# Optimization experiments

Measured on AMD Instinct MI355X. Metric: run time of the kernel, lower is better.

Reference implementation:

```python
import jax, jax.numpy as jnp
import numpy as np

MAX_VAL = 1000000000000.0


def setup_inputs() -> dict:
    key = jax.random.key(0)
    k1, k2, k3, k4 = jax.random.split(key, 4)
    B, H, N, D = 2, 16, 2048, 64
    query = jax.random.normal(k1, (B, H, N, D), dtype=jnp.float32)
    key_t = jax.random.normal(k2, (B, H, N, D), dtype=jnp.float32)
    value = jax.random.normal(k3, (B, H, N, D), dtype=jnp.float32)
    mask = jax.random.randint(k4, (B, 1, 1, N), 0, 2).astype(bool)
    return {"query": query, "key": key_t, "value": value, "mask": mask,
            "global_num": 8, "window_size": 64}


def reference(query, key, value, mask, global_num, window_size):
    # query/key/value: [B, H, N, D]; mask: [B, 1, 1, N] bool (True = keep)
    B, H, N, D = query.shape
    scale = 1.0 / jnp.sqrt(jnp.asarray(D, dtype=query.dtype))

    # split heads: first global_num are global, rest are local (windowed)
    q_g, k_g, v_g = query[:, :global_num], key[:, :global_num], value[:, :global_num]
    q_l, k_l, v_l = query[:, global_num:], key[:, global_num:], value[:, global_num:]

    # ---- global heads: dense masked attention ----
    scores_g = jnp.einsum('bhqd,bhkd->bhqk', q_g, k_g) * scale
    scores_g = jnp.where(mask, scores_g, -MAX_VAL)
    p_g = jax.nn.softmax(scores_g, axis=-1)
    out_g = jnp.einsum('bhqk,bhkd->bhqd', p_g, v_l[:, :0]) if False else jnp.einsum('bhqk,bhkd->bhqd', p_g, v_g)

    # ---- local heads: window-banded mask on top of padding mask ----
    pos = jnp.arange(N)
    distance = jnp.abs(pos[None, :] - pos[:, None])  # [N, N]
    band = (distance <= window_size)                 # [N, N] bool
    mask_l = mask & band                             # [B, 1, N, N]
    scores_l = jnp.einsum('bhqd,bhkd->bhqk', q_l, k_l) * scale
    scores_l = jnp.where(mask_l, scores_l, -MAX_VAL)
    p_l = jax.nn.softmax(scores_l, axis=-1)
    out_l = jnp.einsum('bhqk,bhkd->bhqd', p_l, v_l)

    out = jnp.concatenate([out_g, out_l], axis=1)  # [B, H, N, D]
    return (out, p_g, p_l)
```

## Files before the change

### kernel.cpp

```cpp
#include <hip/hip_runtime.h>
#include <stdint.h>

typedef __attribute__((ext_vector_type(8))) __bf16 bf16x8;
typedef __attribute__((ext_vector_type(4))) float f32x4;
typedef __attribute__((ext_vector_type(4))) int i32x4;

#define DEVI static __device__ __forceinline__

constexpr int NN = 2048;
constexpr int DD = 64;
constexpr int NH = 16;
constexpr int NG = 8;
constexpr float SCALE = 0.125f;
constexpr float NEGBIG = -1.0e12f;
constexpr size_t OUT_ELEMS = (size_t)2 * NH * NN * DD;
constexpr size_t PG_ELEMS  = (size_t)2 * NG * NN * NN;

struct Frag { bf16x8 hi, lo; };

DEVI Frag make_frag(const float* p) {
  f32x4 a = *(const f32x4*)p;
  f32x4 b = *(const f32x4*)(p + 4);
  Frag f;
#pragma unroll
  for (int j = 0; j < 8; j++) {
    float x = (j < 4) ? a[j] : b[j - 4];
    __bf16 h = (__bf16)x;
    f.hi[j] = h;
    f.lo[j] = (__bf16)(x - (float)h);
  }
  return f;
}

DEVI f32x4 mfma(bf16x8 a, bf16x8 b, f32x4 c) {
  return __builtin_amdgcn_mfma_f32_16x16x32_bf16(a, b, c, 0, 0, 0);
}

DEVI void compute_st(const Frag kf[2][2], const Frag* qf_rs, f32x4 acc[2]) {
#pragma unroll
  for (int Mt = 0; Mt < 2; Mt++) {
    f32x4 c = {0.f, 0.f, 0.f, 0.f};
#pragma unroll
    for (int ks = 0; ks < 2; ks++) {
      c = mfma(kf[Mt][ks].hi, qf_rs[ks].hi, c);
      c = mfma(kf[Mt][ks].hi, qf_rs[ks].lo, c);
      c = mfma(kf[Mt][ks].lo, qf_rs[ks].hi, c);
    }
    acc[Mt] = c;
  }
}

__global__ __launch_bounds__(256, 2)
void wattn(const float* __restrict__ Q, const float* __restrict__ K,
           const float* __restrict__ V, const int* __restrict__ MSK,
           float* __restrict__ OUT) {
  const int bid = blockIdx.x;
  const bool loc = bid >= 256;
  const int lb = loc ? bid - 256 : bid;
  const int bh = lb >> 4;
  const int b  = bh >> 3;
  const int hh = bh & 7;
  const int h  = loc ? (hh + 8) : hh;
  const int wave = (int)(threadIdx.x >> 6);
  const int lane = (int)(threadIdx.x & 63);
  const int qi = lane >> 4;
  const int li = lane & 15;
  const int rb = (lb & 15) * 128 + wave * 32;

  const float* qp = Q + ((size_t)(b * NH + h) * NN) * DD;
  const float* kp = K + ((size_t)(b * NH + h) * NN) * DD;
  const float* vp = V + ((size_t)(b * NH + h) * NN) * DD;
  const int*   mp = MSK + (size_t)b * NN;
  float* op = OUT + ((size_t)(b * NH + h) * NN) * DD;
  float* pp = OUT + OUT_ELEMS + (loc ? PG_ELEMS : (size_t)0)
                  + ((size_t)(b * NG + hh) * NN) * NN;

  Frag qf[2][2];
#pragma unroll
  for (int rs = 0; rs < 2; rs++)
#pragma unroll
    for (int ks = 0; ks < 2; ks++)
      qf[rs][ks] = make_frag(qp + (size_t)(rb + rs * 16 + li) * DD + ks * 32 + qi * 8);

  int wlo = 0, whi = 0;
  if (loc) {
    wlo = rb - 64; if (wlo < 0) wlo = 0;
    whi = rb + 96; if (whi > NN) whi = NN;
    const f32x4 z = {0.f, 0.f, 0.f, 0.f};
#pragma unroll 1
    for (int rr = 0; rr < 32; rr++) {
      float* dst = pp + (size_t)(rb + rr) * NN;
#pragma unroll 1
      for (int c = lane * 4; c < NN; c += 256) {
        if (c >= wlo && c < whi) continue;
        *(f32x4*)(dst + c) = z;
      }
    }
  }

  const int ntiles = loc ? 5 : 64;

  float m[2] = {NEGBIG, NEGBIG};
  float l[2] = {0.f, 0.f};

#pragma unroll 1
  for (int t = 0; t < ntiles; t++) {
    const int wc = loc ? (rb - 64 + 32 * t) : (32 * t);
    if (wc < 0 || wc >= NN) continue;

    Frag kf[2][2];
#pragma unroll
    for (int Mt = 0; Mt < 2; Mt++)
#pragma unroll
      for (int ks = 0; ks < 2; ks++)
        kf[Mt][ks] = make_frag(kp + (size_t)(wc + Mt * 16 + li) * DD + ks * 32 + qi * 8);

    i32x4 mv[2];
    mv[0] = *(const i32x4*)(mp + wc + qi * 4);
    mv[1] = *(const i32x4*)(mp + wc + 16 + qi * 4);

#pragma unroll
    for (int rs = 0; rs < 2; rs++) {
      f32x4 acc[2];
      compute_st(kf, qf[rs], acc);
      const int row = rb + rs * 16 + li;
      float vals[8];
#pragma unroll
      for (int Mt = 0; Mt < 2; Mt++)
#pragma unroll
        for (int r = 0; r < 4; r++) {
          const int col = wc + Mt * 16 + qi * 4 + r;
          bool ok = (mv[Mt][r] != 0);
          if (loc) { int d = row - col; if (d < 0) d = -d; ok = ok && (d <= 64); }
          vals[Mt * 4 + r] = ok ? acc[Mt][r] * SCALE : NEGBIG;
        }
      float mx = vals[0];
#pragma unroll
      for (int j = 1; j < 8; j++) mx = fmaxf(mx, vals[j]);
      const float mn = fmaxf(m[rs], mx);
      float s = 0.f;
#pragma unroll
      for (int j = 0; j < 8; j++) s += __expf(vals[j] - mn);
      l[rs] = l[rs] * __expf(m[rs] - mn) + s;
      m[rs] = mn;
    }
  }

  float rl[2];
#pragma unroll
  for (int rs = 0; rs < 2; rs++) {
#pragma unroll
    for (int off = 16; off <= 32; off <<= 1) {
      const float mo = __shfl_xor(m[rs], off);
      const float lo2 = __shfl_xor(l[rs], off);
      const float mn = fmaxf(m[rs], mo);
      l[rs] = l[rs] * __expf(m[rs] - mn) + lo2 * __expf(mo - mn);
      m[rs] = mn;
    }
    rl[rs] = 1.0f / l[rs];
  }

  f32x4 o[2][4];
#pragma unroll
  for (int rs = 0; rs < 2; rs++)
#pragma unroll
    for (int dt = 0; dt < 4; dt++) o[rs][dt] = (f32x4){0.f, 0.f, 0.f, 0.f};

  const int srcA = (((qi * 2) + 0) & 3) * 16 + li;
  const int srcB = (((qi * 2) + 1) & 3) * 16 + li;
  const bool selB = (qi >> 1) != 0;

#pragma unroll 1
  for (int t = 0; t < ntiles; t++) {
    const int wc = loc ? (rb - 64 + 32 * t) : (32 * t);
    if (wc < 0 || wc >= NN) continue;

    Frag kf[2][2];
#pragma unroll
    for (int Mt = 0; Mt < 2; Mt++)
#pragma unroll
      for (int ks = 0; ks < 2; ks++)
        kf[Mt][ks] = make_frag(kp + (size_t)(wc + Mt * 16 + li) * DD + ks * 32 + qi * 8);

    i32x4 mv[2];
    mv[0] = *(const i32x4*)(mp + wc + qi * 4);
    mv[1] = *(const i32x4*)(mp + wc + 16 + qi * 4);

    bf16x8 vf[4];
#pragma unroll
    for (int dt = 0; dt < 4; dt++)
#pragma unroll
      for (int j = 0; j < 8; j++)
        vf[dt][j] = (__bf16)vp[(size_t)(wc + qi * 8 + j) * DD + dt * 16 + li];

#pragma unroll
    for (int rs = 0; rs < 2; rs++) {
      f32x4 acc[2];
      compute_st(kf, qf[rs], acc);
      const int row = rb + rs * 16 + li;
      float pf[8];
#pragma unroll
      for (int Mt = 0; Mt < 2; Mt++)
#pragma unroll
        for (int r = 0; r < 4; r++) {
          const int col = wc + Mt * 16 + qi * 4 + r;
          bool ok = (mv[Mt][r] != 0);
          if (loc) { int d = row - col; if (d < 0) d = -d; ok = ok && (d <= 64); }
          const float vv = ok ? acc[Mt][r] * SCALE : NEGBIG;
          pf[Mt * 4 + r] = __expf(vv - m[rs]) * rl[rs];
        }
      float pa[8];
#pragma unroll
      for (int j = 0; j < 8; j++) {
        const int src = (j < 4) ? srcA : srcB;
        const float v0 = __shfl(pf[0 + (j & 3)], src);
        const float v1 = __shfl(pf[4 + (j & 3)], src);
        pa[j] = selB ? v1 : v0;
      }
      float* prow = pp + (size_t)(rb + rs * 16 + li) * NN + wc + qi * 8;
      *(f32x4*)prow       = (f32x4){pa[0], pa[1], pa[2], pa[3]};
      *(f32x4*)(prow + 4) = (f32x4){pa[4], pa[5], pa[6], pa[7]};
      bf16x8 pb;
#pragma unroll
      for (int j = 0; j < 8; j++) pb[j] = (__bf16)pa[j];
#pragma unroll
      for (int dt = 0; dt < 4; dt++)
        o[rs][dt] = mfma(pb, vf[dt], o[rs][dt]);
    }
  }

#pragma unroll
  for (int rs = 0; rs < 2; rs++) {
#pragma unroll
    for (int dt = 0; dt < 4; dt++)
#pragma unroll
      for (int r = 0; r < 4; r++) {
        const int row = rb + rs * 16 + qi * 4 + r;
        op[(size_t)row * DD + dt * 16 + li] = o[rs][dt][r];
      }
  }
}

extern "C" void kernel_launch(void* const* d_in, const int* in_sizes, int n_in,
                              void* d_out, int out_size, void* d_ws, size_t ws_size,
                              hipStream_t stream) {
  (void)in_sizes; (void)n_in; (void)out_size; (void)d_ws; (void)ws_size;
  const float* Q = (const float*)d_in[0];
  const float* K = (const float*)d_in[1];
  const float* V = (const float*)d_in[2];
  const int*   M = (const int*)d_in[3];
  float* O = (float*)d_out;
  wattn<<<dim3(512), dim3(256), 0, stream>>>(Q, K, V, M, O);
}
```

Measured before the change: 754.5 us.

## Precompute bf16 hi/lo splits of Q/K and transposed bf16 V in workspace

Adds a prep kernel that converts Q and K into separate bf16 hi and lo arrays and writes a transposed bf16 copy of V into the workspace. The attention kernel then loads ready-made fragments with vector loads instead of redoing the float-to-bf16 split for every K tile, and replaces the strided scalar V gathers with contiguous loads. The cost is an extra launch and extra global traffic to write and re-read the workspace. The kernel falls back to the original path when the workspace is too small.

```diff
diff --git a/kernel.cpp b/kernel.cpp
--- a/kernel.cpp
+++ b/kernel.cpp
@@ -15,6 +15,8 @@
 constexpr float NEGBIG = -1.0e12f;
 constexpr size_t OUT_ELEMS = (size_t)2 * NH * NN * DD;
 constexpr size_t PG_ELEMS  = (size_t)2 * NG * NN * NN;
+constexpr size_t T_ELEMS   = (size_t)2 * NH * NN * DD;
+constexpr size_t WS_NEED   = 5 * T_ELEMS * sizeof(__bf16);
 
 struct Frag { bf16x8 hi, lo; };
 
@@ -50,10 +52,50 @@
   }
 }
 
+__global__ __launch_bounds__(256)
+void prep(const float* __restrict__ Q, const float* __restrict__ K,
+          const float* __restrict__ V, __bf16* __restrict__ W) {
+  const int bid = blockIdx.x;
+  if (bid < 4096) {
+    const float* src = (bid < 2048) ? Q : K;
+    __bf16* hi = W + ((bid < 2048) ? (size_t)0 : 2 * T_ELEMS);
+    __bf16* lo = hi + T_ELEMS;
+    const size_t base = ((size_t)(bid & 2047) * 256 + threadIdx.x) * 8;
+    f32x4 a = *(const f32x4*)(src + base);
+    f32x4 b = *(const f32x4*)(src + base + 4);
+    bf16x8 h, l;
+#pragma unroll
+    for (int j = 0; j < 8; j++) {
+      float x = (j < 4) ? a[j] : b[j - 4];
+      __bf16 hh = (__bf16)x;
+      h[j] = hh;
+      l[j] = (__bf16)(x - (float)hh);
+    }
+    *(bf16x8*)(hi + base) = h;
+    *(bf16x8*)(lo + base) = l;
+  } else {
+    __bf16* vt = W + 4 * T_ELEMS;
+    const int t  = (bid - 4096) * 256 + (int)threadIdx.x;
+    const int ng = t & 63;
+    const int dh = t >> 6;
+    const int d  = dh & 63;
+    const int bh = dh >> 6;
+    const float* vp = V + (size_t)bh * NN * DD;
+    __bf16* dst = vt + ((size_t)bh * DD + d) * NN + ng * 32;
+    bf16x8 o[4];
+#pragma unroll
+    for (int j = 0; j < 32; j++)
+      o[j >> 3][j & 7] = (__bf16)vp[(size_t)(ng * 32 + j) * DD + d];
+#pragma unroll
+    for (int k = 0; k < 4; k++) *(bf16x8*)(dst + k * 8) = o[k];
+  }
+}
+
+template <bool PRE>
 __global__ __launch_bounds__(256, 2)
 void wattn(const float* __restrict__ Q, const float* __restrict__ K,
            const float* __restrict__ V, const int* __restrict__ MSK,
-           float* __restrict__ OUT) {
+           float* __restrict__ OUT, const __bf16* __restrict__ W) {
   const int bid = blockIdx.x;
   const bool loc = bid >= 256;
   const int lb = loc ? bid - 256 : bid;
@@ -67,11 +109,17 @@
   const int li = lane & 15;
   const int rb = (lb & 15) * 128 + wave * 32;
 
-  const float* qp = Q + ((size_t)(b * NH + h) * NN) * DD;
-  const float* kp = K + ((size_t)(b * NH + h) * NN) * DD;
-  const float* vp = V + ((size_t)(b * NH + h) * NN) * DD;
+  const size_t tbase = ((size_t)(b * NH + h) * NN) * DD;
+  const float* qp = Q + tbase;
+  const float* kp = K + tbase;
+  const float* vp = V + tbase;
+  const __bf16* qhi = W + tbase;
+  const __bf16* qlo = W + T_ELEMS + tbase;
+  const __bf16* khi = W + 2 * T_ELEMS + tbase;
+  const __bf16* klo = W + 3 * T_ELEMS + tbase;
+  const __bf16* vt  = W + 4 * T_ELEMS + (size_t)(b * NH + h) * DD * NN;
   const int*   mp = MSK + (size_t)b * NN;
-  float* op = OUT + ((size_t)(b * NH + h) * NN) * DD;
+  float* op = OUT + tbase;
   float* pp = OUT + OUT_ELEMS + (loc ? PG_ELEMS : (size_t)0)
                   + ((size_t)(b * NG + hh) * NN) * NN;
 
@@ -79,8 +127,15 @@
 #pragma unroll
   for (int rs = 0; rs < 2; rs++)
 #pragma unroll
-    for (int ks = 0; ks < 2; ks++)
-      qf[rs][ks] = make_frag(qp + (size_t)(rb + rs * 16 + li) * DD + ks * 32 + qi * 8);
+    for (int ks = 0; ks < 2; ks++) {
+      const size_t off = (size_t)(rb + rs * 16 + li) * DD + ks * 32 + qi * 8;
+      if constexpr (PRE) {
+        qf[rs][ks].hi = *(const bf16x8*)(qhi + off);
+        qf[rs][ks].lo = *(const bf16x8*)(qlo + off);
+      } else {
+        qf[rs][ks] = make_frag(qp + off);
+      }
+    }
 
   int wlo = 0, whi = 0;
   if (loc) {
@@ -112,8 +167,15 @@
 #pragma unroll
     for (int Mt = 0; Mt < 2; Mt++)
 #pragma unroll
-      for (int ks = 0; ks < 2; ks++)
-        kf[Mt][ks] = make_frag(kp + (size_t)(wc + Mt * 16 + li) * DD + ks * 32 + qi * 8);
+      for (int ks = 0; ks < 2; ks++) {
+        const size_t off = (size_t)(wc + Mt * 16 + li) * DD + ks * 32 + qi * 8;
+        if constexpr (PRE) {
+          kf[Mt][ks].hi = *(const bf16x8*)(khi + off);
+          kf[Mt][ks].lo = *(const bf16x8*)(klo + off);
+        } else {
+          kf[Mt][ks] = make_frag(kp + off);
+        }
+      }
 
     i32x4 mv[2];
     mv[0] = *(const i32x4*)(mp + wc + qi * 4);
@@ -179,19 +241,32 @@
 #pragma unroll
     for (int Mt = 0; Mt < 2; Mt++)
 #pragma unroll
-      for (int ks = 0; ks < 2; ks++)
-        kf[Mt][ks] = make_frag(kp + (size_t)(wc + Mt * 16 + li) * DD + ks * 32 + qi * 8);
+      for (int ks = 0; ks < 2; ks++) {
+        const size_t off = (size_t)(wc + Mt * 16 + li) * DD + ks * 32 + qi * 8;
+        if constexpr (PRE) {
+          kf[Mt][ks].hi = *(const bf16x8*)(khi + off);
+          kf[Mt][ks].lo = *(const bf16x8*)(klo + off);
+        } else {
+          kf[Mt][ks] = make_frag(kp + off);
+        }
+      }
 
     i32x4 mv[2];
     mv[0] = *(const i32x4*)(mp + wc + qi * 4);
     mv[1] = *(const i32x4*)(mp + wc + 16 + qi * 4);
 
     bf16x8 vf[4];
-#pragma unroll
-    for (int dt = 0; dt < 4; dt++)
-#pragma unroll
-      for (int j = 0; j < 8; j++)
-        vf[dt][j] = (__bf16)vp[(size_t)(wc + qi * 8 + j) * DD + dt * 16 + li];
+    if constexpr (PRE) {
+#pragma unroll
+      for (int dt = 0; dt < 4; dt++)
+        vf[dt] = *(const bf16x8*)(vt + (size_t)(dt * 16 + li) * NN + wc + qi * 8);
+    } else {
+#pragma unroll
+      for (int dt = 0; dt < 4; dt++)
+#pragma unroll
+        for (int j = 0; j < 8; j++)
+          vf[dt][j] = (__bf16)vp[(size_t)(wc + qi * 8 + j) * DD + dt * 16 + li];
+    }
 
 #pragma unroll
     for (int rs = 0; rs < 2; rs++) {
@@ -244,11 +319,17 @@
 extern "C" void kernel_launch(void* const* d_in, const int* in_sizes, int n_in,
                               void* d_out, int out_size, void* d_ws, size_t ws_size,
                               hipStream_t stream) {
-  (void)in_sizes; (void)n_in; (void)out_size; (void)d_ws; (void)ws_size;
+  (void)in_sizes; (void)n_in; (void)out_size;
   const float* Q = (const float*)d_in[0];
   const float* K = (const float*)d_in[1];
   const float* V = (const float*)d_in[2];
   const int*   M = (const int*)d_in[3];
   float* O = (float*)d_out;
-  wattn<<<dim3(512), dim3(256), 0, stream>>>(Q, K, V, M, O);
-}
+  if (ws_size >= WS_NEED && d_ws != nullptr) {
+    __bf16* W = (__bf16*)d_ws;
+    prep<<<dim3(4608), dim3(256), 0, stream>>>(Q, K, V, W);
+    wattn<true><<<dim3(512), dim3(256), 0, stream>>>(Q, K, V, M, O, W);
+  } else {
+    wattn<false><<<dim3(512), dim3(256), 0, stream>>>(Q, K, V, M, O, nullptr);
+  }
+}
```

New measurement: 784.0 us. +3.9%, slower.

## Balance global and local head work per wave with 16-row jobs

Applied to the files above, without the earlier changes.

Each wave now handles 16 query rows instead of 32, and runs one global-head job followed by one local-head job for the same (b, head-index, rows), so every block carries equal work instead of separate light local blocks and heavy global blocks. Block IDs are remapped so consecutive blocks land on different XCDs. The local-head zero fill of the probability matrix moves into the second pass loop as tile-wise stores, which replaces the separate per-row strided zeroing. Halving rows per wave doubles the K/V fragment loads per query row, which raises global load traffic.

```diff
diff --git a/kernel.cpp b/kernel.cpp
--- a/kernel.cpp
+++ b/kernel.cpp
@@ -36,209 +36,190 @@
   return __builtin_amdgcn_mfma_f32_16x16x32_bf16(a, b, c, 0, 0, 0);
 }
 
-DEVI void compute_st(const Frag kf[2][2], const Frag* qf_rs, f32x4 acc[2]) {
+DEVI void compute_st(const Frag kf[2][2], const Frag qf[2], f32x4 acc[2]) {
 #pragma unroll
   for (int Mt = 0; Mt < 2; Mt++) {
     f32x4 c = {0.f, 0.f, 0.f, 0.f};
 #pragma unroll
     for (int ks = 0; ks < 2; ks++) {
-      c = mfma(kf[Mt][ks].hi, qf_rs[ks].hi, c);
-      c = mfma(kf[Mt][ks].hi, qf_rs[ks].lo, c);
-      c = mfma(kf[Mt][ks].lo, qf_rs[ks].hi, c);
+      c = mfma(kf[Mt][ks].hi, qf[ks].hi, c);
+      c = mfma(kf[Mt][ks].hi, qf[ks].lo, c);
+      c = mfma(kf[Mt][ks].lo, qf[ks].hi, c);
     }
     acc[Mt] = c;
   }
+}
+
+template <bool LOC>
+DEVI void attn_job(int bh, int r0, int lane,
+                   const float* __restrict__ Q, const float* __restrict__ K,
+                   const float* __restrict__ V, const int* __restrict__ MSK,
+                   float* __restrict__ OUT) {
+  const int b  = bh >> 3;
+  const int hh = bh & 7;
+  const int h  = LOC ? (hh + 8) : hh;
+  const int qi = lane >> 4;
+  const int li = lane & 15;
+
+  const size_t tb = ((size_t)(b * NH + h) * NN) * DD;
+  const float* qp = Q + tb;
+  const float* kp = K + tb;
+  const float* vp = V + tb;
+  const int*   mp = MSK + (size_t)b * NN;
+  float* op = OUT + tb;
+  float* pp = OUT + OUT_ELEMS + (LOC ? PG_ELEMS : (size_t)0)
+                  + ((size_t)(b * NG + hh) * NN) * NN;
+
+  Frag qf[2];
+#pragma unroll
+  for (int ks = 0; ks < 2; ks++)
+    qf[ks] = make_frag(qp + (size_t)(r0 + li) * DD + ks * 32 + qi * 8);
+
+  int cb = 0;
+  if constexpr (LOC) cb = (r0 - 64) & ~31;
+
+  float m = NEGBIG, l = 0.f;
+
+  const int ntA = LOC ? 5 : 64;
+#pragma unroll 1
+  for (int t = 0; t < ntA; t++) {
+    const int wc = LOC ? (cb + 32 * t) : (32 * t);
+    if (LOC && ((unsigned)wc >= (unsigned)NN)) continue;
+
+    Frag kf[2][2];
+#pragma unroll
+    for (int Mt = 0; Mt < 2; Mt++)
+#pragma unroll
+      for (int ks = 0; ks < 2; ks++)
+        kf[Mt][ks] = make_frag(kp + (size_t)(wc + Mt * 16 + li) * DD + ks * 32 + qi * 8);
+
+    i32x4 mv[2];
+    mv[0] = *(const i32x4*)(mp + wc + qi * 4);
+    mv[1] = *(const i32x4*)(mp + wc + 16 + qi * 4);
+
+    f32x4 acc[2];
+    compute_st(kf, qf, acc);
+    const int row = r0 + li;
+    float vals[8];
+#pragma unroll
+    for (int Mt = 0; Mt < 2; Mt++)
+#pragma unroll
+      for (int r = 0; r < 4; r++) {
+        const int col = wc + Mt * 16 + qi * 4 + r;
+        bool ok = (mv[Mt][r] != 0);
+        if constexpr (LOC) { int d = row - col; if (d < 0) d = -d; ok = ok && (d <= 64); }
+        vals[Mt * 4 + r] = ok ? acc[Mt][r] * SCALE : NEGBIG;
+      }
+    float mx = vals[0];
+#pragma unroll
+    for (int j = 1; j < 8; j++) mx = fmaxf(mx, vals[j]);
+    const float mn = fmaxf(m, mx);
+    float s = 0.f;
+#pragma unroll
+    for (int j = 0; j < 8; j++) s += __expf(vals[j] - mn);
+    l = l * __expf(m - mn) + s;
+    m = mn;
+  }
+
+#pragma unroll
+  for (int off = 16; off <= 32; off <<= 1) {
+    const float mo  = __shfl_xor(m, off);
+    const float lo2 = __shfl_xor(l, off);
+    const float mn  = fmaxf(m, mo);
+    l = l * __expf(m - mn) + lo2 * __expf(mo - mn);
+    m = mn;
+  }
+  const float rl = 1.0f / l;
+
+  f32x4 o[4];
+#pragma unroll
+  for (int dt = 0; dt < 4; dt++) o[dt] = (f32x4){0.f, 0.f, 0.f, 0.f};
+
+  const int srcA = (((qi * 2) + 0) & 3) * 16 + li;
+  const int srcB = (((qi * 2) + 1) & 3) * 16 + li;
+  const bool selB = (qi >> 1) != 0;
+
+#pragma unroll 1
+  for (int t = 0; t < 64; t++) {
+    const int wc = 32 * t;
+    float* prow = pp + (size_t)(r0 + li) * NN + wc + qi * 8;
+    if (LOC && ((unsigned)(wc - cb) >= 160u)) {
+      const f32x4 z = {0.f, 0.f, 0.f, 0.f};
+      *(f32x4*)prow       = z;
+      *(f32x4*)(prow + 4) = z;
+      continue;
+    }
+
+    Frag kf[2][2];
+#pragma unroll
+    for (int Mt = 0; Mt < 2; Mt++)
+#pragma unroll
+      for (int ks = 0; ks < 2; ks++)
+        kf[Mt][ks] = make_frag(kp + (size_t)(wc + Mt * 16 + li) * DD + ks * 32 + qi * 8);
+
+    i32x4 mv[2];
+    mv[0] = *(const i32x4*)(mp + wc + qi * 4);
+    mv[1] = *(const i32x4*)(mp + wc + 16 + qi * 4);
+
+    bf16x8 vf[4];
+#pragma unroll
+    for (int dt = 0; dt < 4; dt++)
+#pragma unroll
+      for (int j = 0; j < 8; j++)
+        vf[dt][j] = (__bf16)vp[(size_t)(wc + qi * 8 + j) * DD + dt * 16 + li];
+
+    f32x4 acc[2];
+    compute_st(kf, qf, acc);
+    const int row = r0 + li;
+    float pf[8];
+#pragma unroll
+    for (int Mt = 0; Mt < 2; Mt++)
+#pragma unroll
+      for (int r = 0; r < 4; r++) {
+        const int col = wc + Mt * 16 + qi * 4 + r;
+        bool ok = (mv[Mt][r] != 0);
+        if constexpr (LOC) { int d = row - col; if (d < 0) d = -d; ok = ok && (d <= 64); }
+        const float vv = ok ? acc[Mt][r] * SCALE : NEGBIG;
+        pf[Mt * 4 + r] = __expf(vv - m) * rl;
+      }
+    float pa[8];
+#pragma unroll
+    for (int j = 0; j < 8; j++) {
+      const int src = (j < 4) ? srcA : srcB;
+      const float v0 = __shfl(pf[0 + (j & 3)], src);
+      const float v1 = __shfl(pf[4 + (j & 3)], src);
+      pa[j] = selB ? v1 : v0;
+    }
+    *(f32x4*)prow       = (f32x4){pa[0], pa[1], pa[2], pa[3]};
+    *(f32x4*)(prow + 4) = (f32x4){pa[4], pa[5], pa[6], pa[7]};
+    bf16x8 pb;
+#pragma unroll
+    for (int j = 0; j < 8; j++) pb[j] = (__bf16)pa[j];
+#pragma unroll
+    for (int dt = 0; dt < 4; dt++)
+      o[dt] = mfma(pb, vf[dt], o[dt]);
+  }
+
+#pragma unroll
+  for (int dt = 0; dt < 4; dt++)
+#pragma unroll
+    for (int r = 0; r < 4; r++)
+      op[(size_t)(r0 + qi * 4 + r) * DD + dt * 16 + li] = o[dt][r];
 }
 
 __global__ __launch_bounds__(256, 2)
 void wattn(const float* __restrict__ Q, const float* __restrict__ K,
            const float* __restrict__ V, const int* __restrict__ MSK,
            float* __restrict__ OUT) {
-  const int bid = blockIdx.x;
-  const bool loc = bid >= 256;
-  const int lb = loc ? bid - 256 : bid;
-  const int bh = lb >> 4;
-  const int b  = bh >> 3;
-  const int hh = bh & 7;
-  const int h  = loc ? (hh + 8) : hh;
   const int wave = (int)(threadIdx.x >> 6);
   const int lane = (int)(threadIdx.x & 63);
-  const int qi = lane >> 4;
-  const int li = lane & 15;
-  const int rb = (lb & 15) * 128 + wave * 32;
-
-  const float* qp = Q + ((size_t)(b * NH + h) * NN) * DD;
-  const float* kp = K + ((size_t)(b * NH + h) * NN) * DD;
-  const float* vp = V + ((size_t)(b * NH + h) * NN) * DD;
-  const int*   mp = MSK + (size_t)b * NN;
-  float* op = OUT + ((size_t)(b * NH + h) * NN) * DD;
-  float* pp = OUT + OUT_ELEMS + (loc ? PG_ELEMS : (size_t)0)
-                  + ((size_t)(b * NG + hh) * NN) * NN;
-
-  Frag qf[2][2];
-#pragma unroll
-  for (int rs = 0; rs < 2; rs++)
-#pragma unroll
-    for (int ks = 0; ks < 2; ks++)
-      qf[rs][ks] = make_frag(qp + (size_t)(rb + rs * 16 + li) * DD + ks * 32 + qi * 8);
-
-  int wlo = 0, whi = 0;
-  if (loc) {
-    wlo = rb - 64; if (wlo < 0) wlo = 0;
-    whi = rb + 96; if (whi > NN) whi = NN;
-    const f32x4 z = {0.f, 0.f, 0.f, 0.f};
-#pragma unroll 1
-    for (int rr = 0; rr < 32; rr++) {
-      float* dst = pp + (size_t)(rb + rr) * NN;
-#pragma unroll 1
-      for (int c = lane * 4; c < NN; c += 256) {
-        if (c >= wlo && c < whi) continue;
-        *(f32x4*)(dst + c) = z;
-      }
-    }
-  }
-
-  const int ntiles = loc ? 5 : 64;
-
-  float m[2] = {NEGBIG, NEGBIG};
-  float l[2] = {0.f, 0.f};
-
-#pragma unroll 1
-  for (int t = 0; t < ntiles; t++) {
-    const int wc = loc ? (rb - 64 + 32 * t) : (32 * t);
-    if (wc < 0 || wc >= NN) continue;
-
-    Frag kf[2][2];
-#pragma unroll
-    for (int Mt = 0; Mt < 2; Mt++)
-#pragma unroll
-      for (int ks = 0; ks < 2; ks++)
-        kf[Mt][ks] = make_frag(kp + (size_t)(wc + Mt * 16 + li) * DD + ks * 32 + qi * 8);
-
-    i32x4 mv[2];
-    mv[0] = *(const i32x4*)(mp + wc + qi * 4);
-    mv[1] = *(const i32x4*)(mp + wc + 16 + qi * 4);
-
-#pragma unroll
-    for (int rs = 0; rs < 2; rs++) {
-      f32x4 acc[2];
-      compute_st(kf, qf[rs], acc);
-      const int row = rb + rs * 16 + li;
-      float vals[8];
-#pragma unroll
-      for (int Mt = 0; Mt < 2; Mt++)
-#pragma unroll
-        for (int r = 0; r < 4; r++) {
-          const int col = wc + Mt * 16 + qi * 4 + r;
-          bool ok = (mv[Mt][r] != 0);
-          if (loc) { int d = row - col; if (d < 0) d = -d; ok = ok && (d <= 64); }
-          vals[Mt * 4 + r] = ok ? acc[Mt][r] * SCALE : NEGBIG;
-        }
-      float mx = vals[0];
-#pragma unroll
-      for (int j = 1; j < 8; j++) mx = fmaxf(mx, vals[j]);
-      const float mn = fmaxf(m[rs], mx);
-      float s = 0.f;
-#pragma unroll
-      for (int j = 0; j < 8; j++) s += __expf(vals[j] - mn);
-      l[rs] = l[rs] * __expf(m[rs] - mn) + s;
-      m[rs] = mn;
-    }
-  }
-
-  float rl[2];
-#pragma unroll
-  for (int rs = 0; rs < 2; rs++) {
-#pragma unroll
-    for (int off = 16; off <= 32; off <<= 1) {
-      const float mo = __shfl_xor(m[rs], off);
-      const float lo2 = __shfl_xor(l[rs], off);
-      const float mn = fmaxf(m[rs], mo);
-      l[rs] = l[rs] * __expf(m[rs] - mn) + lo2 * __expf(mo - mn);
-      m[rs] = mn;
-    }
-    rl[rs] = 1.0f / l[rs];
-  }
-
-  f32x4 o[2][4];
-#pragma unroll
-  for (int rs = 0; rs < 2; rs++)
-#pragma unroll
-    for (int dt = 0; dt < 4; dt++) o[rs][dt] = (f32x4){0.f, 0.f, 0.f, 0.f};
-
-  const int srcA = (((qi * 2) + 0) & 3) * 16 + li;
-  const int srcB = (((qi * 2) + 1) & 3) * 16 + li;
-  const bool selB = (qi >> 1) != 0;
-
-#pragma unroll 1
-  for (int t = 0; t < ntiles; t++) {
-    const int wc = loc ? (rb - 64 + 32 * t) : (32 * t);
-    if (wc < 0 || wc >= NN) continue;
-
-    Frag kf[2][2];
-#pragma unroll
-    for (int Mt = 0; Mt < 2; Mt++)
-#pragma unroll
-      for (int ks = 0; ks < 2; ks++)
-        kf[Mt][ks] = make_frag(kp + (size_t)(wc + Mt * 16 + li) * DD + ks * 32 + qi * 8);
-
-    i32x4 mv[2];
-    mv[0] = *(const i32x4*)(mp + wc + qi * 4);
-    mv[1] = *(const i32x4*)(mp + wc + 16 + qi * 4);
-
-    bf16x8 vf[4];
-#pragma unroll
-    for (int dt = 0; dt < 4; dt++)
-#pragma unroll
-      for (int j = 0; j < 8; j++)
-        vf[dt][j] = (__bf16)vp[(size_t)(wc + qi * 8 + j) * DD + dt * 16 + li];
-
-#pragma unroll
-    for (int rs = 0; rs < 2; rs++) {
-      f32x4 acc[2];
-      compute_st(kf, qf[rs], acc);
-      const int row = rb + rs * 16 + li;
-      float pf[8];
-#pragma unroll
-      for (int Mt = 0; Mt < 2; Mt++)
-#pragma unroll
-        for (int r = 0; r < 4; r++) {
-          const int col = wc + Mt * 16 + qi * 4 + r;
-          bool ok = (mv[Mt][r] != 0);
-          if (loc) { int d = row - col; if (d < 0) d = -d; ok = ok && (d <= 64); }
-          const float vv = ok ? acc[Mt][r] * SCALE : NEGBIG;
-          pf[Mt * 4 + r] = __expf(vv - m[rs]) * rl[rs];
-        }
-      float pa[8];
-#pragma unroll
-      for (int j = 0; j < 8; j++) {
-        const int src = (j < 4) ? srcA : srcB;
-        const float v0 = __shfl(pf[0 + (j & 3)], src);
-        const float v1 = __shfl(pf[4 + (j & 3)], src);
-        pa[j] = selB ? v1 : v0;
-      }
-      float* prow = pp + (size_t)(rb + rs * 16 + li) * NN + wc + qi * 8;
-      *(f32x4*)prow       = (f32x4){pa[0], pa[1], pa[2], pa[3]};
-      *(f32x4*)(prow + 4) = (f32x4){pa[4], pa[5], pa[6], pa[7]};
-      bf16x8 pb;
-#pragma unroll
-      for (int j = 0; j < 8; j++) pb[j] = (__bf16)pa[j];
-#pragma unroll
-      for (int dt = 0; dt < 4; dt++)
-        o[rs][dt] = mfma(pb, vf[dt], o[rs][dt]);
-    }
-  }
-
-#pragma unroll
-  for (int rs = 0; rs < 2; rs++) {
-#pragma unroll
-    for (int dt = 0; dt < 4; dt++)
-#pragma unroll
-      for (int r = 0; r < 4; r++) {
-        const int row = rb + rs * 16 + qi * 4 + r;
-        op[(size_t)row * DD + dt * 16 + li] = o[rs][dt][r];
-      }
-  }
+  const int sb = ((int)blockIdx.x & 7) * 64 + ((int)blockIdx.x >> 3);
+  const int gw = sb * 4 + wave;
+  const int bh = gw >> 7;
+  const int r0 = (gw & 127) * 16;
+
+  attn_job<false>(bh, r0, lane, Q, K, V, MSK, OUT);
+  attn_job<true >(bh, r0, lane, Q, K, V, MSK, OUT);
 }
 
 extern "C" void kernel_launch(void* const* d_in, const int* in_sizes, int n_in,
```

After: 866.6 us. 1.15x slower.
